# Optimization experiments

Measured on AMD Instinct MI355X. Metric: run time of the kernel, lower is better.

## Reference

```python
import jax, jax.numpy as jnp
import numpy as np

W_POSE, W_MATCH, W_EPI = 1.0, 0.5, 0.1
EPS = 1e-8


def setup_inputs() -> dict:
    key = jax.random.key(0)
    ks = jax.random.split(key, 8)
    B, N, M = 16, 1024, 1024
    R_pred = jax.random.normal(ks[0], (B, 3, 3), dtype=jnp.float32)
    t_pred = jax.random.normal(ks[1], (B, 3), dtype=jnp.float32)
    R_gt = jax.random.normal(ks[2], (B, 3, 3), dtype=jnp.float32)
    t_gt = jax.random.normal(ks[3], (B, 3), dtype=jnp.float32)
    # realistic invertible camera intrinsics + small randn perturbation
    K_base = jnp.array([[500.0, 0.0, 320.0], [0.0, 500.0, 240.0], [0.0, 0.0, 1.0]], dtype=jnp.float32)
    K = K_base[None] + 0.01 * jax.random.normal(ks[4], (B, 3, 3), dtype=jnp.float32)
    kp1 = jax.random.normal(ks[5], (B, N, 2), dtype=jnp.float32)
    kp2 = jax.random.normal(ks[6], (B, N, 2), dtype=jnp.float32)
    matches = jax.random.uniform(ks[7], (B, N, M), dtype=jnp.float32)
    return {"R_pred": R_pred, "t_pred": t_pred, "R_gt": R_gt, "t_gt": t_gt,
            "K": K, "kp1": kp1, "kp2": kp2, "matches": matches}


def _homo(pts):
    # [B,N,2] -> [B,N,3]
    return jnp.concatenate([pts, jnp.ones(pts.shape[:-1] + (1,), pts.dtype)], axis=-1)


def _masked_weighted_mean(errors, matches):
    # samples with <3 surviving pairs are skipped (mirrors torch.where + skip).
    thr = jnp.max(matches, axis=(1, 2), keepdims=True) * 0.1
    mask = matches > thr
    w = jnp.where(mask, matches, 0.0)
    count = jnp.sum(mask, axis=(1, 2))
    valid = count >= 3
    per_b = jnp.sum(errors * w, axis=(1, 2)) / (jnp.sum(w, axis=(1, 2)) + EPS)
    per_b = jnp.where(valid, per_b, 0.0)
    n_valid = jnp.sum(valid)
    return jnp.where(n_valid > 0, jnp.sum(per_b) / jnp.maximum(n_valid, 1), 0.0)


def _fundamental(R, t, K):
    t_n = t / jnp.linalg.norm(t, axis=1, keepdims=True)  # F.normalize p=2 dim=1
    z = jnp.zeros_like(t_n[:, 0])
    t_skew = jnp.stack([
        jnp.stack([z, -t_n[:, 2], t_n[:, 1]], axis=-1),
        jnp.stack([t_n[:, 2], z, -t_n[:, 0]], axis=-1),
        jnp.stack([-t_n[:, 1], t_n[:, 0], z], axis=-1),
    ], axis=1)  # [B,3,3]
    E = jnp.einsum('bij,bjk->bik', t_skew, R)
    K_inv = jnp.linalg.inv(K)
    return jnp.einsum('bji,bjk,bkl->bil', K_inv, E, K_inv)  # K_inv^T E K_inv


def reference(R_pred, t_pred, R_gt, t_gt, K, kp1, kp2, matches):
    # rotation loss
    trace = jnp.einsum('bij,bij->b', R_pred, R_gt)  # trace(R_pred @ R_gt^T)
    geodesic = jnp.clip((trace - 1.0) / 2.0, -1.0 + 1e-7, 1.0 - 1e-7)
    rot_loss = jnp.mean(1.0 - geodesic)
    # translation loss
    t_gt_n = t_gt / jnp.linalg.norm(t_gt, axis=1, keepdims=True)
    trans_loss = jnp.mean(1.0 - jnp.sum(t_pred * t_gt_n, axis=1))
    pose_loss = rot_loss + trans_loss

    pts1_h = _homo(kp1)  # [B,N,3]
    pts2_h = _homo(kp2)  # [B,M,3]

    # correspondence loss: transformed pts1 by R_gt, error vs every kp2 -> [B,N,M]
    T = jnp.einsum('bij,bnj->bni', R_gt, pts1_h)[..., :2]  # [B,N,2]
    diff = kp2[:, None, :, :] - T[:, :, None, :]           # [B,N,M,2]
    corr_err = jnp.linalg.norm(diff, axis=-1)              # [B,N,M]
    match_loss = _masked_weighted_mean(corr_err, matches)

    # epipolar loss: |pts2_h[j]^T F pts1_h[i]| -> [B,N,M] indexed (i,j)
    F_mat = _fundamental(R_gt, t_gt, K)
    A = jnp.einsum('bmk,bkl->bml', pts2_h, F_mat)          # [B,M,3]
    epi_err = jnp.abs(jnp.einsum('bml,bnl->bnm', A, pts1_h))
    epi_loss = _masked_weighted_mean(epi_err, matches)

    total = W_POSE * pose_loss + W_MATCH * match_loss + W_EPI * epi_loss
    return total
```

## Files before the change

kernel.cpp:

```cpp
#include <hip/hip_runtime.h>

#define B 16
#define N 1024
#define M 1024
#define TN 8
#define NBLK (B * (N / TN))

#define WS_PMAX  0
#define WS_ROT   2048
#define WS_TRANS 2064
#define WS_THR   2080
#define WS_PACC  2112
#define WS_T     10304
#define WS_A     43072

__launch_bounds__(256, 8)
__global__ void k_max(const float* __restrict__ matches, float* __restrict__ ws) {
    int bid = blockIdx.x;
    int t = threadIdx.x;
    const float4* m4 = (const float4*)matches + (long)bid * (TN * (M / 4)) + t;
    float4 d[TN];
    #pragma unroll
    for (int n = 0; n < TN; ++n) d[n] = m4[n * (M / 4)];
    float v = 0.f;
    #pragma unroll
    for (int n = 0; n < TN; ++n)
        v = fmaxf(v, fmaxf(fmaxf(d[n].x, d[n].y), fmaxf(d[n].z, d[n].w)));
    #pragma unroll
    for (int off = 32; off; off >>= 1) v = fmaxf(v, __shfl_down(v, off));
    __shared__ float sm[4];
    if ((t & 63) == 0) sm[t >> 6] = v;
    __syncthreads();
    if (t == 0)
        ws[WS_PMAX + bid] = fmaxf(fmaxf(sm[0], sm[1]), fmaxf(sm[2], sm[3]));
}

__global__ void k_prep(const float* __restrict__ R_pred, const float* __restrict__ t_pred,
                       const float* __restrict__ R_gt,   const float* __restrict__ t_gt,
                       const float* __restrict__ K, const float* __restrict__ kp1,
                       const float* __restrict__ kp2, float* __restrict__ ws) {
    int b = blockIdx.x;
    int t = threadIdx.x;
    __shared__ float sF[9];

    if (t < 64) {
        float pv = fmaxf(ws[WS_PMAX + b*128 + t], ws[WS_PMAX + b*128 + 64 + t]);
        #pragma unroll
        for (int off = 32; off; off >>= 1) pv = fmaxf(pv, __shfl_down(pv, off));
        if (t == 0) ws[WS_THR + b] = 0.1f * pv;
    }

    if (t == 0) {
        const float* Rp = R_pred + b*9;
        const float* Rg = R_gt   + b*9;
        float trace = 0.f;
        #pragma unroll
        for (int i = 0; i < 9; ++i) trace += Rp[i] * Rg[i];
        float geo = (trace - 1.f) * 0.5f;
        geo = fminf(fmaxf(geo, -1.f + 1e-7f), 1.f - 1e-7f);
        ws[WS_ROT + b] = 1.f - geo;

        const float* tg = t_gt + b*3;
        const float* tp = t_pred + b*3;
        float nrm = sqrtf(tg[0]*tg[0] + tg[1]*tg[1] + tg[2]*tg[2]);
        float tx = tg[0]/nrm, ty = tg[1]/nrm, tz = tg[2]/nrm;
        ws[WS_TRANS + b] = 1.f - (tp[0]*tx + tp[1]*ty + tp[2]*tz);

        float E[3][3];
        #pragma unroll
        for (int c = 0; c < 3; ++c) {
            E[0][c] = -tz*Rg[3+c] + ty*Rg[6+c];
            E[1][c] =  tz*Rg[0+c] - tx*Rg[6+c];
            E[2][c] = -ty*Rg[0+c] + tx*Rg[3+c];
        }
        const float* Km = K + b*9;
        float m00=Km[0], m01=Km[1], m02=Km[2];
        float m10=Km[3], m11=Km[4], m12=Km[5];
        float m20=Km[6], m21=Km[7], m22=Km[8];
        float c00 =  (m11*m22 - m12*m21);
        float c01 = -(m10*m22 - m12*m20);
        float c02 =  (m10*m21 - m11*m20);
        float c10 = -(m01*m22 - m02*m21);
        float c11 =  (m00*m22 - m02*m20);
        float c12 = -(m00*m21 - m01*m20);
        float c20 =  (m01*m12 - m02*m11);
        float c21 = -(m00*m12 - m02*m10);
        float c22 =  (m00*m11 - m01*m10);
        float det = m00*c00 + m01*c01 + m02*c02;
        float id = 1.f / det;
        float Ki[3][3] = {{c00*id, c10*id, c20*id},
                          {c01*id, c11*id, c21*id},
                          {c02*id, c12*id, c22*id}};
        float Tmp[3][3];
        #pragma unroll
        for (int j = 0; j < 3; ++j)
            #pragma unroll
            for (int l = 0; l < 3; ++l)
                Tmp[j][l] = E[j][0]*Ki[0][l] + E[j][1]*Ki[1][l] + E[j][2]*Ki[2][l];
        #pragma unroll
        for (int i = 0; i < 3; ++i)
            #pragma unroll
            for (int l = 0; l < 3; ++l)
                sF[i*3 + l] = Ki[0][i]*Tmp[0][l] + Ki[1][i]*Tmp[1][l] + Ki[2][i]*Tmp[2][l];
    }
    __syncthreads();

    const float* Rg = R_gt + b*9;
    float2* T = (float2*)(ws + WS_T) + b*N;
    float* A = ws + WS_A + b*3*M;
    for (int n = t; n < N; n += 256) {
        float x = kp1[(b*N + n)*2 + 0], y = kp1[(b*N + n)*2 + 1];
        float2 r;
        r.x = Rg[0]*x + Rg[1]*y + Rg[2];
        r.y = Rg[3]*x + Rg[4]*y + Rg[5];
        T[n] = r;
    }
    for (int m = t; m < M; m += 256) {
        float x = kp2[(b*M + m)*2 + 0], y = kp2[(b*M + m)*2 + 1];
        A[m]       = sF[0]*x + sF[3]*y + sF[6];
        A[M + m]   = sF[1]*x + sF[4]*y + sF[7];
        A[2*M + m] = sF[2]*x + sF[5]*y + sF[8];
    }
}

__launch_bounds__(256, 4)
__global__ void k_main(const float* __restrict__ matches, const float* __restrict__ kp1,
                       const float* __restrict__ kp2, float* __restrict__ ws) {
    int bid  = blockIdx.x;
    int b    = bid >> 7;
    int n0   = (bid & 127) * TN;
    int t    = threadIdx.x;
    int w    = t >> 6, lane = t & 63;

    const float4* m4 = (const float4*)matches + (long)bid * (TN * (M / 4)) + t;
    float4 d[TN];
    #pragma unroll
    for (int n = 0; n < TN; ++n) d[n] = m4[n * (M / 4)];

    __shared__ float2 sT[TN], sP[TN];
    if (t < TN) sT[t] = ((const float2*)(ws + WS_T))[b*N + n0 + t];
    if (t >= 64 && t < 64 + TN) {
        int i = t - 64;
        sP[i] = ((const float2*)kp1)[(long)b*N + n0 + i];
    }

    const float4* kp2v = (const float4*)(kp2 + b*M*2);
    float4 q0 = kp2v[t*2], q1 = kp2v[t*2 + 1];
    float k2x[4] = {q0.x, q0.z, q1.x, q1.z};
    float k2y[4] = {q0.y, q0.w, q1.y, q1.w};
    const float4* Av = (const float4*)(ws + WS_A + b*3*M);
    float4 a0 = Av[t], a1 = Av[M/4 + t], a2 = Av[2*(M/4) + t];
    float A0[4] = {a0.x, a0.y, a0.z, a0.w};
    float A1[4] = {a1.x, a1.y, a1.z, a1.w};
    float A2[4] = {a2.x, a2.y, a2.z, a2.w};

    float thr = ws[WS_THR + b];
    __syncthreads();

    float s_w = 0.f, s_c = 0.f, s_e = 0.f, s_n = 0.f;
    #pragma unroll
    for (int n = 0; n < TN; ++n) {
        float Tx = sT[n].x, Ty = sT[n].y, px = sP[n].x, py = sP[n].y;
        float mvv[4] = {d[n].x, d[n].y, d[n].z, d[n].w};
        #pragma unroll
        for (int j = 0; j < 4; ++j) {
            float wgt = mvv[j];
            bool pass = wgt > thr;
            float ww = pass ? wgt : 0.f;
            s_n += pass ? 1.f : 0.f;
            float dx = k2x[j] - Tx, dy = k2y[j] - Ty;
            float ce = sqrtf(dx*dx + dy*dy);
            float ee = fabsf(A0[j]*px + A1[j]*py + A2[j]);
            s_w += ww;
            s_c += ce * ww;
            s_e += ee * ww;
        }
    }
    #pragma unroll
    for (int off = 32; off; off >>= 1) {
        s_w += __shfl_down(s_w, off);
        s_c += __shfl_down(s_c, off);
        s_e += __shfl_down(s_e, off);
        s_n += __shfl_down(s_n, off);
    }
    __shared__ float4 pacc[4];
    if (lane == 0) pacc[w] = make_float4(s_w, s_c, s_e, s_n);
    __syncthreads();
    if (t == 0) {
        float4 r = pacc[0];
        #pragma unroll
        for (int i = 1; i < 4; ++i) {
            r.x += pacc[i].x; r.y += pacc[i].y; r.z += pacc[i].z; r.w += pacc[i].w;
        }
        ((float4*)(ws + WS_PACC))[bid] = r;
    }
}

__global__ void k_final(const float* __restrict__ ws, float* __restrict__ out) {
    int t = threadIdx.x;
    int b = t >> 4, i = t & 15;
    float4 acc = make_float4(0.f, 0.f, 0.f, 0.f);
    const float4* pacc = (const float4*)(ws + WS_PACC);
    for (int j = i; j < 128; j += 16) {
        float4 r = pacc[b*128 + j];
        acc.x += r.x; acc.y += r.y; acc.z += r.z; acc.w += r.w;
    }
    #pragma unroll
    for (int off = 8; off; off >>= 1) {
        acc.x += __shfl_down(acc.x, off);
        acc.y += __shfl_down(acc.y, off);
        acc.z += __shfl_down(acc.z, off);
        acc.w += __shfl_down(acc.w, off);
    }
    __shared__ float4 sb[16];
    if (i == 0) sb[b] = acc;
    __syncthreads();
    if (t == 0) {
        float rot = 0.f, tr = 0.f, ms = 0.f, es = 0.f;
        int nv = 0;
        for (int bb = 0; bb < B; ++bb) {
            rot += ws[WS_ROT + bb];
            tr  += ws[WS_TRANS + bb];
            float4 r = sb[bb];
            if (r.w >= 3.f) { nv++; ms += r.y / (r.x + 1e-8f); es += r.z / (r.x + 1e-8f); }
        }
        float match = nv > 0 ? ms / (float)nv : 0.f;
        float epi   = nv > 0 ? es / (float)nv : 0.f;
        out[0] = (rot + tr) * (1.f / (float)B) + 0.5f * match + 0.1f * epi;
    }
}

extern "C" void kernel_launch(void* const* d_in, const int* in_sizes, int n_in,
                              void* d_out, int out_size, void* d_ws, size_t ws_size,
                              hipStream_t stream) {
    const float* R_pred  = (const float*)d_in[0];
    const float* t_pred  = (const float*)d_in[1];
    const float* R_gt    = (const float*)d_in[2];
    const float* t_gt    = (const float*)d_in[3];
    const float* K       = (const float*)d_in[4];
    const float* kp1     = (const float*)d_in[5];
    const float* kp2     = (const float*)d_in[6];
    const float* matches = (const float*)d_in[7];
    float* out = (float*)d_out;
    float* ws  = (float*)d_ws;

    k_max <<<NBLK, 256, 0, stream>>>(matches, ws);
    k_prep<<<B,    256, 0, stream>>>(R_pred, t_pred, R_gt, t_gt, K, kp1, kp2, ws);
    k_main<<<NBLK, 256, 0, stream>>>(matches, kp1, kp2, ws);
    k_final<<<1,   256, 0, stream>>>(ws, out);
}
```

Before: 45.09 us.

## Single-pass matches read with block-local threshold and band correction kernel

Merges the max, prep and main kernels into one pass that reads the matches tensor once. Each block accumulates using its own local 0.1*max threshold and stores the few elements that fall just above that threshold in a small band buffer. A second kernel then subtracts the band elements that fall below the global per-sample threshold, and re-reads the block's matches only when the band overflows or the global threshold lies above the band cap. A last-block atomic counter performs the final reduction and pose loss, removing two launches. This saves a full pass over the large tensor in the common case but adds scan and band-write work, and falls back to re-reading matches when the local and global maxima differ a lot.

```diff
diff --git a/kernel.cpp b/kernel.cpp
--- a/kernel.cpp
+++ b/kernel.cpp
@@ -5,175 +5,121 @@
 #define M 1024
 #define TN 8
 #define NBLK (B * (N / TN))
-
-#define WS_PMAX  0
-#define WS_ROT   2048
-#define WS_TRANS 2064
-#define WS_THR   2080
+#define C2 64
+
+#define WS_CNTR  0
+#define WS_PMAX  64
 #define WS_PACC  2112
-#define WS_T     10304
-#define WS_A     43072
-
-__launch_bounds__(256, 8)
-__global__ void k_max(const float* __restrict__ matches, float* __restrict__ ws) {
-    int bid = blockIdx.x;
-    int t = threadIdx.x;
-    const float4* m4 = (const float4*)matches + (long)bid * (TN * (M / 4)) + t;
+#define WS_BCNT  10304
+#define WS_BAND  12352
+
+#define NEG_INF (-3.402823466e+38f)
+
+__device__ __forceinline__ void compute_F(const float* __restrict__ Rgp,
+                                          const float* __restrict__ tg,
+                                          const float* __restrict__ Km,
+                                          float* F)
+{
+    float m00=Km[0], m01=Km[1], m02=Km[2];
+    float m10=Km[3], m11=Km[4], m12=Km[5];
+    float m20=Km[6], m21=Km[7], m22=Km[8];
+    float c00 =  (m11*m22 - m12*m21), c01 = -(m10*m22 - m12*m20), c02 =  (m10*m21 - m11*m20);
+    float c10 = -(m01*m22 - m02*m21), c11 =  (m00*m22 - m02*m20), c12 = -(m00*m21 - m01*m20);
+    float c20 =  (m01*m12 - m02*m11), c21 = -(m00*m12 - m02*m10), c22 =  (m00*m11 - m01*m10);
+    float id  = 1.f / (m00*c00 + m01*c01 + m02*c02);
+    float Ki00 = c00*id, Ki01 = c10*id, Ki02 = c20*id;
+    float Ki10 = c01*id, Ki11 = c11*id, Ki12 = c21*id;
+    float Ki20 = c02*id, Ki21 = c12*id, Ki22 = c22*id;
+    float inr = rsqrtf(tg[0]*tg[0] + tg[1]*tg[1] + tg[2]*tg[2]);
+    float tx = tg[0]*inr, ty = tg[1]*inr, tz = tg[2]*inr;
+    float Rg0=Rgp[0],Rg1=Rgp[1],Rg2=Rgp[2],Rg3=Rgp[3],Rg4=Rgp[4],Rg5=Rgp[5],Rg6=Rgp[6],Rg7=Rgp[7],Rg8=Rgp[8];
+    float E00=-tz*Rg3+ty*Rg6, E01=-tz*Rg4+ty*Rg7, E02=-tz*Rg5+ty*Rg8;
+    float E10= tz*Rg0-tx*Rg6, E11= tz*Rg1-tx*Rg7, E12= tz*Rg2-tx*Rg8;
+    float E20=-ty*Rg0+tx*Rg3, E21=-ty*Rg1+tx*Rg4, E22=-ty*Rg2+tx*Rg5;
+    float T00=E00*Ki00+E01*Ki10+E02*Ki20, T01=E00*Ki01+E01*Ki11+E02*Ki21, T02=E00*Ki02+E01*Ki12+E02*Ki22;
+    float T10=E10*Ki00+E11*Ki10+E12*Ki20, T11=E10*Ki01+E11*Ki11+E12*Ki21, T12=E10*Ki02+E11*Ki12+E12*Ki22;
+    float T20=E20*Ki00+E21*Ki10+E22*Ki20, T21=E20*Ki01+E21*Ki11+E22*Ki21, T22=E20*Ki02+E21*Ki12+E22*Ki22;
+    F[0]=Ki00*T00+Ki10*T10+Ki20*T20; F[1]=Ki00*T01+Ki10*T11+Ki20*T21; F[2]=Ki00*T02+Ki10*T12+Ki20*T22;
+    F[3]=Ki01*T00+Ki11*T10+Ki21*T20; F[4]=Ki01*T01+Ki11*T11+Ki21*T21; F[5]=Ki01*T02+Ki11*T12+Ki21*T22;
+    F[6]=Ki02*T00+Ki12*T10+Ki22*T20; F[7]=Ki02*T01+Ki12*T11+Ki22*T21; F[8]=Ki02*T02+Ki12*T12+Ki22*T22;
+}
+
+__launch_bounds__(256, 4)
+__global__ void k1_fused(const float* __restrict__ matches,
+                         const float* __restrict__ R_gt, const float* __restrict__ t_gt,
+                         const float* __restrict__ Kin,
+                         const float* __restrict__ kp1,  const float* __restrict__ kp2,
+                         float* __restrict__ ws)
+{
+    const int bid = blockIdx.x;
+    const int b = bid >> 7;
+    const int row0 = (bid & 127) * TN;
+    const int t = threadIdx.x;
+    const int lane = t & 63, wv = t >> 6;
+    if (bid == 0 && t == 0) ((unsigned int*)ws)[WS_CNTR] = 0u;
+
+    __shared__ float4 sTP[TN];
+    __shared__ float  sm[4];
+    __shared__ float4 paccL[4];
+    __shared__ int    wtot[4];
+
+    const float4* m4 = (const float4*)matches + ((long)b * N + row0) * (M/4) + t;
     float4 d[TN];
     #pragma unroll
-    for (int n = 0; n < TN; ++n) d[n] = m4[n * (M / 4)];
-    float v = 0.f;
+    for (int n = 0; n < TN; ++n) d[n] = m4[n * (M/4)];
+
+    const float* Rgp = R_gt + b * 9;
+    if (t < TN) {
+        float2 p = ((const float2*)kp1)[(long)b * N + row0 + t];
+        sTP[t] = make_float4(Rgp[0]*p.x + Rgp[1]*p.y + Rgp[2],
+                             Rgp[3]*p.x + Rgp[4]*p.y + Rgp[5], p.x, p.y);
+    }
+
+    float F[9];
+    compute_F(Rgp, t_gt + b*3, Kin + b*9, F);
+    const float4* kp2v = (const float4*)(kp2 + (long)b * M * 2);
+    float4 q0 = kp2v[2*t], q1 = kp2v[2*t + 1];
+    float k2x[4] = {q0.x, q0.z, q1.x, q1.z};
+    float k2y[4] = {q0.y, q0.w, q1.y, q1.w};
+    float A0[4], A1[4], A2[4];
+    #pragma unroll
+    for (int j = 0; j < 4; ++j) {
+        A0[j] = k2x[j]*F[0] + k2y[j]*F[3] + F[6];
+        A1[j] = k2x[j]*F[1] + k2y[j]*F[4] + F[7];
+        A2[j] = k2x[j]*F[2] + k2y[j]*F[5] + F[8];
+    }
+    __syncthreads();
+
+    float v = NEG_INF;
     #pragma unroll
     for (int n = 0; n < TN; ++n)
         v = fmaxf(v, fmaxf(fmaxf(d[n].x, d[n].y), fmaxf(d[n].z, d[n].w)));
     #pragma unroll
     for (int off = 32; off; off >>= 1) v = fmaxf(v, __shfl_down(v, off));
-    __shared__ float sm[4];
-    if ((t & 63) == 0) sm[t >> 6] = v;
-    __syncthreads();
-    if (t == 0)
-        ws[WS_PMAX + bid] = fmaxf(fmaxf(sm[0], sm[1]), fmaxf(sm[2], sm[3]));
-}
-
-__global__ void k_prep(const float* __restrict__ R_pred, const float* __restrict__ t_pred,
-                       const float* __restrict__ R_gt,   const float* __restrict__ t_gt,
-                       const float* __restrict__ K, const float* __restrict__ kp1,
-                       const float* __restrict__ kp2, float* __restrict__ ws) {
-    int b = blockIdx.x;
-    int t = threadIdx.x;
-    __shared__ float sF[9];
-
-    if (t < 64) {
-        float pv = fmaxf(ws[WS_PMAX + b*128 + t], ws[WS_PMAX + b*128 + 64 + t]);
-        #pragma unroll
-        for (int off = 32; off; off >>= 1) pv = fmaxf(pv, __shfl_down(pv, off));
-        if (t == 0) ws[WS_THR + b] = 0.1f * pv;
-    }
-
-    if (t == 0) {
-        const float* Rp = R_pred + b*9;
-        const float* Rg = R_gt   + b*9;
-        float trace = 0.f;
-        #pragma unroll
-        for (int i = 0; i < 9; ++i) trace += Rp[i] * Rg[i];
-        float geo = (trace - 1.f) * 0.5f;
-        geo = fminf(fmaxf(geo, -1.f + 1e-7f), 1.f - 1e-7f);
-        ws[WS_ROT + b] = 1.f - geo;
-
-        const float* tg = t_gt + b*3;
-        const float* tp = t_pred + b*3;
-        float nrm = sqrtf(tg[0]*tg[0] + tg[1]*tg[1] + tg[2]*tg[2]);
-        float tx = tg[0]/nrm, ty = tg[1]/nrm, tz = tg[2]/nrm;
-        ws[WS_TRANS + b] = 1.f - (tp[0]*tx + tp[1]*ty + tp[2]*tz);
-
-        float E[3][3];
-        #pragma unroll
-        for (int c = 0; c < 3; ++c) {
-            E[0][c] = -tz*Rg[3+c] + ty*Rg[6+c];
-            E[1][c] =  tz*Rg[0+c] - tx*Rg[6+c];
-            E[2][c] = -ty*Rg[0+c] + tx*Rg[3+c];
-        }
-        const float* Km = K + b*9;
-        float m00=Km[0], m01=Km[1], m02=Km[2];
-        float m10=Km[3], m11=Km[4], m12=Km[5];
-        float m20=Km[6], m21=Km[7], m22=Km[8];
-        float c00 =  (m11*m22 - m12*m21);
-        float c01 = -(m10*m22 - m12*m20);
-        float c02 =  (m10*m21 - m11*m20);
-        float c10 = -(m01*m22 - m02*m21);
-        float c11 =  (m00*m22 - m02*m20);
-        float c12 = -(m00*m21 - m01*m20);
-        float c20 =  (m01*m12 - m02*m11);
-        float c21 = -(m00*m12 - m02*m10);
-        float c22 =  (m00*m11 - m01*m10);
-        float det = m00*c00 + m01*c01 + m02*c02;
-        float id = 1.f / det;
-        float Ki[3][3] = {{c00*id, c10*id, c20*id},
-                          {c01*id, c11*id, c21*id},
-                          {c02*id, c12*id, c22*id}};
-        float Tmp[3][3];
-        #pragma unroll
-        for (int j = 0; j < 3; ++j)
-            #pragma unroll
-            for (int l = 0; l < 3; ++l)
-                Tmp[j][l] = E[j][0]*Ki[0][l] + E[j][1]*Ki[1][l] + E[j][2]*Ki[2][l];
-        #pragma unroll
-        for (int i = 0; i < 3; ++i)
-            #pragma unroll
-            for (int l = 0; l < 3; ++l)
-                sF[i*3 + l] = Ki[0][i]*Tmp[0][l] + Ki[1][i]*Tmp[1][l] + Ki[2][i]*Tmp[2][l];
-    }
-    __syncthreads();
-
-    const float* Rg = R_gt + b*9;
-    float2* T = (float2*)(ws + WS_T) + b*N;
-    float* A = ws + WS_A + b*3*M;
-    for (int n = t; n < N; n += 256) {
-        float x = kp1[(b*N + n)*2 + 0], y = kp1[(b*N + n)*2 + 1];
-        float2 r;
-        r.x = Rg[0]*x + Rg[1]*y + Rg[2];
-        r.y = Rg[3]*x + Rg[4]*y + Rg[5];
-        T[n] = r;
-    }
-    for (int m = t; m < M; m += 256) {
-        float x = kp2[(b*M + m)*2 + 0], y = kp2[(b*M + m)*2 + 1];
-        A[m]       = sF[0]*x + sF[3]*y + sF[6];
-        A[M + m]   = sF[1]*x + sF[4]*y + sF[7];
-        A[2*M + m] = sF[2]*x + sF[5]*y + sF[8];
-    }
-}
-
-__launch_bounds__(256, 4)
-__global__ void k_main(const float* __restrict__ matches, const float* __restrict__ kp1,
-                       const float* __restrict__ kp2, float* __restrict__ ws) {
-    int bid  = blockIdx.x;
-    int b    = bid >> 7;
-    int n0   = (bid & 127) * TN;
-    int t    = threadIdx.x;
-    int w    = t >> 6, lane = t & 63;
-
-    const float4* m4 = (const float4*)matches + (long)bid * (TN * (M / 4)) + t;
-    float4 d[TN];
-    #pragma unroll
-    for (int n = 0; n < TN; ++n) d[n] = m4[n * (M / 4)];
-
-    __shared__ float2 sT[TN], sP[TN];
-    if (t < TN) sT[t] = ((const float2*)(ws + WS_T))[b*N + n0 + t];
-    if (t >= 64 && t < 64 + TN) {
-        int i = t - 64;
-        sP[i] = ((const float2*)kp1)[(long)b*N + n0 + i];
-    }
-
-    const float4* kp2v = (const float4*)(kp2 + b*M*2);
-    float4 q0 = kp2v[t*2], q1 = kp2v[t*2 + 1];
-    float k2x[4] = {q0.x, q0.z, q1.x, q1.z};
-    float k2y[4] = {q0.y, q0.w, q1.y, q1.w};
-    const float4* Av = (const float4*)(ws + WS_A + b*3*M);
-    float4 a0 = Av[t], a1 = Av[M/4 + t], a2 = Av[2*(M/4) + t];
-    float A0[4] = {a0.x, a0.y, a0.z, a0.w};
-    float A1[4] = {a1.x, a1.y, a1.z, a1.w};
-    float A2[4] = {a2.x, a2.y, a2.z, a2.w};
-
-    float thr = ws[WS_THR + b];
-    __syncthreads();
+    if (lane == 0) sm[wv] = v;
+    __syncthreads();
+    float bmax = fmaxf(fmaxf(sm[0], sm[1]), fmaxf(sm[2], sm[3]));
+    if (t == 0) ws[WS_PMAX + bid] = bmax;
+    float thr_b = 0.1f * bmax;
+    float cap_b = 1.01f * thr_b;
 
     float s_w = 0.f, s_c = 0.f, s_e = 0.f, s_n = 0.f;
+    int bcnt = 0;
     #pragma unroll
     for (int n = 0; n < TN; ++n) {
-        float Tx = sT[n].x, Ty = sT[n].y, px = sP[n].x, py = sP[n].y;
-        float mvv[4] = {d[n].x, d[n].y, d[n].z, d[n].w};
+        float4 tp = sTP[n];
+        float mv[4] = {d[n].x, d[n].y, d[n].z, d[n].w};
         #pragma unroll
         for (int j = 0; j < 4; ++j) {
-            float wgt = mvv[j];
-            bool pass = wgt > thr;
-            float ww = pass ? wgt : 0.f;
+            float w = mv[j];
+            bool pass = w > thr_b;
+            float ww = pass ? w : 0.f;
             s_n += pass ? 1.f : 0.f;
-            float dx = k2x[j] - Tx, dy = k2y[j] - Ty;
+            bcnt += (pass && w <= cap_b) ? 1 : 0;
+            float dx = k2x[j] - tp.x, dy = k2y[j] - tp.y;
             float ce = sqrtf(dx*dx + dy*dy);
-            float ee = fabsf(A0[j]*px + A1[j]*py + A2[j]);
-            s_w += ww;
-            s_c += ce * ww;
-            s_e += ee * ww;
+            float ee = fabsf(A0[j]*tp.z + A1[j]*tp.w + A2[j]);
+            s_w += ww; s_c += ce*ww; s_e += ee*ww;
         }
     }
     #pragma unroll
@@ -183,50 +129,219 @@
         s_e += __shfl_down(s_e, off);
         s_n += __shfl_down(s_n, off);
     }
-    __shared__ float4 pacc[4];
-    if (lane == 0) pacc[w] = make_float4(s_w, s_c, s_e, s_n);
+    int incl = bcnt;
+    #pragma unroll
+    for (int off = 1; off < 64; off <<= 1) {
+        int y = __shfl_up(incl, off);
+        if (lane >= off) incl += y;
+    }
+    if (lane == 0)  paccL[wv] = make_float4(s_w, s_c, s_e, s_n);
+    if (lane == 63) wtot[wv] = incl;
     __syncthreads();
     if (t == 0) {
-        float4 r = pacc[0];
-        #pragma unroll
-        for (int i = 1; i < 4; ++i) {
-            r.x += pacc[i].x; r.y += pacc[i].y; r.z += pacc[i].z; r.w += pacc[i].w;
-        }
+        float4 r = paccL[0];
+        #pragma unroll
+        for (int i = 1; i < 4; ++i) { r.x += paccL[i].x; r.y += paccL[i].y; r.z += paccL[i].z; r.w += paccL[i].w; }
         ((float4*)(ws + WS_PACC))[bid] = r;
     }
+    int pos = incl - bcnt;
+    #pragma unroll
+    for (int k = 0; k < 4; ++k) if (k < wv) pos += wtot[k];
+    int total = wtot[0] + wtot[1] + wtot[2] + wtot[3];
+    if (t == 0) ((unsigned int*)ws)[WS_BCNT + bid] = (unsigned int)total;
+
+    if (total > 0 && total <= C2) {
+        float* band = ws + WS_BAND + (long)bid * (C2 * 3);
+        #pragma unroll
+        for (int n = 0; n < TN; ++n) {
+            float4 tp = sTP[n];
+            float mv[4] = {d[n].x, d[n].y, d[n].z, d[n].w};
+            #pragma unroll
+            for (int j = 0; j < 4; ++j) {
+                float w = mv[j];
+                if (w > thr_b && w <= cap_b) {
+                    float dx = k2x[j] - tp.x, dy = k2y[j] - tp.y;
+                    float ce = sqrtf(dx*dx + dy*dy);
+                    float ee = fabsf(A0[j]*tp.z + A1[j]*tp.w + A2[j]);
+                    band[pos*3 + 0] = w;
+                    band[pos*3 + 1] = ce * w;
+                    band[pos*3 + 2] = ee * w;
+                    ++pos;
+                }
+            }
+        }
+    }
 }
 
-__global__ void k_final(const float* __restrict__ ws, float* __restrict__ out) {
-    int t = threadIdx.x;
-    int b = t >> 4, i = t & 15;
-    float4 acc = make_float4(0.f, 0.f, 0.f, 0.f);
-    const float4* pacc = (const float4*)(ws + WS_PACC);
-    for (int j = i; j < 128; j += 16) {
-        float4 r = pacc[b*128 + j];
-        acc.x += r.x; acc.y += r.y; acc.z += r.z; acc.w += r.w;
-    }
-    #pragma unroll
-    for (int off = 8; off; off >>= 1) {
-        acc.x += __shfl_down(acc.x, off);
-        acc.y += __shfl_down(acc.y, off);
-        acc.z += __shfl_down(acc.z, off);
-        acc.w += __shfl_down(acc.w, off);
-    }
-    __shared__ float4 sb[16];
-    if (i == 0) sb[b] = acc;
-    __syncthreads();
+__launch_bounds__(256, 4)
+__global__ void k2_fix(const float* __restrict__ matches,
+                       const float* __restrict__ R_pred, const float* __restrict__ t_pred,
+                       const float* __restrict__ R_gt,   const float* __restrict__ t_gt,
+                       const float* __restrict__ Kin,
+                       const float* __restrict__ kp1,    const float* __restrict__ kp2,
+                       float* __restrict__ ws, float* __restrict__ out)
+{
+    const int bid = blockIdx.x;
+    const int b = bid >> 7;
+    const int row0 = (bid & 127) * TN;
+    const int t = threadIdx.x;
+    const int lane = t & 63, wv = t >> 6;
+
+    __shared__ float  sThr;
+    __shared__ int    sLast;
+    __shared__ float4 sTP[TN];
+    __shared__ float4 paccL[4];
+
+    if (t < 64) {
+        float pv = fmaxf(ws[WS_PMAX + b*128 + t], ws[WS_PMAX + b*128 + 64 + t]);
+        #pragma unroll
+        for (int off = 32; off; off >>= 1) pv = fmaxf(pv, __shfl_down(pv, off));
+        if (t == 0) sThr = 0.1f * pv;
+    }
+    __syncthreads();
+    const float thr = sThr;
+
+    float bmax  = ws[WS_PMAX + bid];
+    float thr_b = 0.1f * bmax;
+    float cap_b = 1.01f * thr_b;
+    unsigned int bcnt = ((const unsigned int*)ws)[WS_BCNT + bid];
+    bool reread = (bcnt > C2) || (thr > cap_b);
+
+    if (!reread) {
+        float c_w = 0.f, c_c = 0.f, c_e = 0.f, c_n = 0.f;
+        if (t < (int)bcnt) {
+            const float* band = ws + WS_BAND + (long)bid * (C2 * 3);
+            float w = band[t*3 + 0];
+            if (!(w > thr)) {
+                c_w = w; c_c = band[t*3 + 1]; c_e = band[t*3 + 2]; c_n = 1.f;
+            }
+        }
+        if (wv == 0) {
+            #pragma unroll
+            for (int off = 32; off; off >>= 1) {
+                c_w += __shfl_down(c_w, off);
+                c_c += __shfl_down(c_c, off);
+                c_e += __shfl_down(c_e, off);
+                c_n += __shfl_down(c_n, off);
+            }
+        }
+        if (t == 0) {
+            float4 p = ((const float4*)(ws + WS_PACC))[bid];
+            ((float4*)(ws + WS_PACC))[bid] = make_float4(p.x - c_w, p.y - c_c, p.z - c_e, p.w - c_n);
+        }
+    } else {
+        const float* Rgp = R_gt + b * 9;
+        if (t < TN) {
+            float2 p = ((const float2*)kp1)[(long)b * N + row0 + t];
+            sTP[t] = make_float4(Rgp[0]*p.x + Rgp[1]*p.y + Rgp[2],
+                                 Rgp[3]*p.x + Rgp[4]*p.y + Rgp[5], p.x, p.y);
+        }
+        float F[9];
+        compute_F(Rgp, t_gt + b*3, Kin + b*9, F);
+        const float4* kp2v = (const float4*)(kp2 + (long)b * M * 2);
+        float4 q0 = kp2v[2*t], q1 = kp2v[2*t + 1];
+        float k2x[4] = {q0.x, q0.z, q1.x, q1.z};
+        float k2y[4] = {q0.y, q0.w, q1.y, q1.w};
+        float A0[4], A1[4], A2[4];
+        #pragma unroll
+        for (int j = 0; j < 4; ++j) {
+            A0[j] = k2x[j]*F[0] + k2y[j]*F[3] + F[6];
+            A1[j] = k2x[j]*F[1] + k2y[j]*F[4] + F[7];
+            A2[j] = k2x[j]*F[2] + k2y[j]*F[5] + F[8];
+        }
+        const float4* m4 = (const float4*)matches + ((long)b * N + row0) * (M/4) + t;
+        float4 d[TN];
+        #pragma unroll
+        for (int n = 0; n < TN; ++n) d[n] = m4[n * (M/4)];
+        __syncthreads();
+        float s_w = 0.f, s_c = 0.f, s_e = 0.f, s_n = 0.f;
+        #pragma unroll
+        for (int n = 0; n < TN; ++n) {
+            float4 tp = sTP[n];
+            float mv[4] = {d[n].x, d[n].y, d[n].z, d[n].w};
+            #pragma unroll
+            for (int j = 0; j < 4; ++j) {
+                float w = mv[j];
+                bool pass = w > thr;
+                float ww = pass ? w : 0.f;
+                s_n += pass ? 1.f : 0.f;
+                float dx = k2x[j] - tp.x, dy = k2y[j] - tp.y;
+                float ce = sqrtf(dx*dx + dy*dy);
+                float ee = fabsf(A0[j]*tp.z + A1[j]*tp.w + A2[j]);
+                s_w += ww; s_c += ce*ww; s_e += ee*ww;
+            }
+        }
+        #pragma unroll
+        for (int off = 32; off; off >>= 1) {
+            s_w += __shfl_down(s_w, off);
+            s_c += __shfl_down(s_c, off);
+            s_e += __shfl_down(s_e, off);
+            s_n += __shfl_down(s_n, off);
+        }
+        if (lane == 0) paccL[wv] = make_float4(s_w, s_c, s_e, s_n);
+        __syncthreads();
+        if (t == 0) {
+            float4 r = paccL[0];
+            #pragma unroll
+            for (int i = 1; i < 4; ++i) { r.x += paccL[i].x; r.y += paccL[i].y; r.z += paccL[i].z; r.w += paccL[i].w; }
+            ((float4*)(ws + WS_PACC))[bid] = r;
+        }
+    }
+
     if (t == 0) {
-        float rot = 0.f, tr = 0.f, ms = 0.f, es = 0.f;
+        __threadfence();
+        unsigned int old = atomicAdd(((unsigned int*)ws) + WS_CNTR, 1u);
+        sLast = (old == (unsigned int)(NBLK - 1)) ? 1 : 0;
+    }
+    __syncthreads();
+    if (!sLast) return;
+    __threadfence();
+
+    __shared__ float4 sAcc[B];
+    __shared__ float  sPose[B];
+    if (t < B) {
+        const float* Rp = R_pred + t * 9;
+        const float* Rq = R_gt   + t * 9;
+        float trace = 0.f;
+        #pragma unroll
+        for (int i = 0; i < 9; ++i) trace += Rp[i] * Rq[i];
+        float geo = fminf(fmaxf((trace - 1.f) * 0.5f, -1.f + 1e-7f), 1.f - 1e-7f);
+        const float* tq = t_gt   + t * 3;
+        const float* tp = t_pred + t * 3;
+        float in2 = rsqrtf(tq[0]*tq[0] + tq[1]*tq[1] + tq[2]*tq[2]);
+        float dotp = (tp[0]*tq[0] + tp[1]*tq[1] + tp[2]*tq[2]) * in2;
+        sPose[t] = (1.f - geo) + (1.f - dotp);
+    }
+    {
+        int b2 = t >> 4, i = t & 15;
+        const float4* pa = (const float4*)(ws + WS_PACC);
+        float4 acc = make_float4(0.f, 0.f, 0.f, 0.f);
+        #pragma unroll
+        for (int j = 0; j < 8; ++j) {
+            float4 r = pa[b2*128 + i + j*16];
+            acc.x += r.x; acc.y += r.y; acc.z += r.z; acc.w += r.w;
+        }
+        #pragma unroll
+        for (int off = 8; off; off >>= 1) {
+            acc.x += __shfl_down(acc.x, off);
+            acc.y += __shfl_down(acc.y, off);
+            acc.z += __shfl_down(acc.z, off);
+            acc.w += __shfl_down(acc.w, off);
+        }
+        if (i == 0) sAcc[b2] = acc;
+    }
+    __syncthreads();
+    if (t == 0) {
+        float pose = 0.f, ms = 0.f, es = 0.f;
         int nv = 0;
         for (int bb = 0; bb < B; ++bb) {
-            rot += ws[WS_ROT + bb];
-            tr  += ws[WS_TRANS + bb];
-            float4 r = sb[bb];
+            pose += sPose[bb];
+            float4 r = sAcc[bb];
             if (r.w >= 3.f) { nv++; ms += r.y / (r.x + 1e-8f); es += r.z / (r.x + 1e-8f); }
         }
         float match = nv > 0 ? ms / (float)nv : 0.f;
         float epi   = nv > 0 ? es / (float)nv : 0.f;
-        out[0] = (rot + tr) * (1.f / (float)B) + 0.5f * match + 0.1f * epi;
+        out[0] = pose * (1.f / (float)B) + 0.5f * match + 0.1f * epi;
     }
 }
 
@@ -244,8 +359,6 @@
     float* out = (float*)d_out;
     float* ws  = (float*)d_ws;
 
-    k_max <<<NBLK, 256, 0, stream>>>(matches, ws);
-    k_prep<<<B,    256, 0, stream>>>(R_pred, t_pred, R_gt, t_gt, K, kp1, kp2, ws);
-    k_main<<<NBLK, 256, 0, stream>>>(matches, kp1, kp2, ws);
-    k_final<<<1,   256, 0, stream>>>(ws, out);
+    k1_fused<<<NBLK, 256, 0, stream>>>(matches, R_gt, t_gt, K, kp1, kp2, ws);
+    k2_fix  <<<NBLK, 256, 0, stream>>>(matches, R_pred, t_pred, R_gt, t_gt, K, kp1, kp2, ws, out);
 }
```

After: 76.42 us. 69.5% more time.
